# Kernel tuning notes

Hardware: AMD Instinct MI355X
Metric: run time of the kernel (lower is better)

The kernel has to match this reference:

```python
import jax, jax.numpy as jnp
import numpy as np

E = 256  # embed_dim (hardcoded in source module)
H = 4    # n_head
D = E // H
SEQ = 32768


def setup_inputs() -> dict:
    key = jax.random.key(0)
    ks = jax.random.split(key, 5)
    x = jax.random.normal(ks[0], (SEQ, E), dtype=jnp.float32)
    in_proj_weight = jax.random.normal(ks[1], (3 * E, E), dtype=jnp.float32) * (1.0 / np.sqrt(E))
    in_proj_bias = jax.random.normal(ks[2], (3 * E,), dtype=jnp.float32) * 0.02
    out_proj_weight = jax.random.normal(ks[3], (E, E), dtype=jnp.float32) * (1.0 / np.sqrt(E))
    out_proj_bias = jax.random.normal(ks[4], (E,), dtype=jnp.float32) * 0.02
    return {
        "x": x,
        "in_proj_weight": in_proj_weight,
        "in_proj_bias": in_proj_bias,
        "out_proj_weight": out_proj_weight,
        "out_proj_bias": out_proj_bias,
    }


def reference(x, in_proj_weight, in_proj_bias, out_proj_weight, out_proj_bias):
    # QKV projections (q uses only the first token of x: single-query decode attention)
    Wq, Wk, Wv = in_proj_weight[:E], in_proj_weight[E:2 * E], in_proj_weight[2 * E:]
    bq, bk, bv = in_proj_bias[:E], in_proj_bias[E:2 * E], in_proj_bias[2 * E:]
    q = x[:1] @ Wq.T + bq            # [1, E]
    k = x @ Wk.T + bk                # [S, E]
    v = x @ Wv.T + bv                # [S, E]

    qh = q.reshape(H, D)             # [H, D] (single query)
    kh = k.reshape(-1, H, D)         # [S, H, D]
    vh = v.reshape(-1, H, D)         # [S, H, D]

    scale = 1.0 / np.sqrt(D).astype(np.float32)
    scores = jnp.einsum("hd,shd->hs", qh, kh) * scale   # [H, S]
    attn = jax.nn.softmax(scores, axis=-1)                # [H, S]
    ctx = jnp.einsum("hs,shd->hd", attn, vh)             # [H, D]

    out = ctx.reshape(1, E) @ out_proj_weight.T + out_proj_bias  # [1, E]
    return out
```

## Files before the change

kernel.cpp:

```cpp
#include <hip/hip_runtime.h>
#include <hip/hip_cooperative_groups.h>
namespace cg = cooperative_groups;

#define NBLK 272
#define NB_B 256
#define WS_LP   0
#define WS_YV   1024
#define WS_B2   2048
#define WS_KQ   2304
#define WS_C4   3328
#define WS_M2   3392
#define WS_YP   265536

__device__ __forceinline__ float dot4(float4 a, float4 b) {
  return a.x * b.x + a.y * b.y + a.z * b.z + a.w * b.w;
}

__device__ __forceinline__ void phaseA_kq(const float* __restrict__ x, const float* __restrict__ W,
                                          const float* __restrict__ inb, float* __restrict__ kq,
                                          float* __restrict__ c4, float* sh, int ab, int t) {
  float* xs = sh;
  float* qls = sh + 256;
  float* red = sh + 320;
  const int lane = t & 63, w = t >> 6;
  const int h = ab >> 2, qt = ab & 3;
  if (t < 256) xs[t] = x[t];
  __syncthreads();
  const float4 xv = *(const float4*)&xs[lane * 4];
#pragma unroll
  for (int k = 0; k < 8; ++k) {
    const int eloc = w * 8 + k;
    const int row = h * 64 + eloc;
    float4 wv = *(const float4*)&W[(size_t)row * 256 + lane * 4];
    float p = dot4(wv, xv);
#pragma unroll
    for (int m = 1; m < 64; m <<= 1) p += __shfl_xor(p, m);
    if (lane == 0) qls[eloc] = p + inb[row];
  }
  __syncthreads();
  const int cl = t & 63, ds = t >> 6;
  float acc = 0.f;
#pragma unroll
  for (int d2 = 0; d2 < 8; ++d2) {
    const int d = ds * 8 + d2;
    acc += W[(size_t)(256 + h * 64 + d) * 256 + qt * 64 + cl] * qls[d];
  }
  red[ds * 64 + cl] = acc;
  __syncthreads();
  if (ds == 0) {
    float s = 0.f;
#pragma unroll
    for (int i = 0; i < 8; ++i) s += red[i * 64 + cl];
    kq[h * 256 + qt * 64 + cl] = s;
  }
  if (qt == 0 && t < 64) {
    float v = qls[t] * inb[256 + h * 64 + t];
#pragma unroll
    for (int m = 1; m < 64; m <<= 1) v += __shfl_xor(v, m);
    if (t == 0) c4[h] = v;
  }
}

__device__ __forceinline__ void phaseA_m2(const float* __restrict__ W, const float* __restrict__ Wout,
                                          float* __restrict__ M2, float* sh, int b2, int t) {
  float* wout_t = sh;
  const int tile = b2 >> 1, sub = b2 & 1;
  const int h = tile >> 4, e0 = (tile & 15) * 16 + sub * 8;
  {
    const int e = t >> 6, d = t & 63;
    wout_t[e * 64 + d] = Wout[(size_t)(e0 + e) * 256 + h * 64 + d];
  }
  __syncthreads();
  const int c = t & 255, eh = t >> 8;
  float acc[4] = {0.f, 0.f, 0.f, 0.f};
#pragma unroll 8
  for (int d = 0; d < 64; ++d) {
    const float wv = W[(size_t)(512 + h * 64 + d) * 256 + c];
#pragma unroll
    for (int e = 0; e < 4; ++e) acc[e] += wv * wout_t[(eh * 4 + e) * 64 + d];
  }
#pragma unroll
  for (int e = 0; e < 4; ++e)
    M2[(size_t)(e0 + eh * 4 + e) * 1024 + h * 256 + c] = acc[e];
}

__device__ __forceinline__ void phaseA_b2(const float* __restrict__ Wout, const float* __restrict__ inb,
                                          const float* __restrict__ bout, float* __restrict__ bias2,
                                          float* sh, int b, int t) {
  float* red = sh;
  const int og = t >> 5, seg = t & 31;
  const int e = b * 16 + og;
  float acc = 0.f;
#pragma unroll
  for (int j = 0; j < 8; ++j)
    acc += Wout[(size_t)e * 256 + seg * 8 + j] * inb[512 + seg * 8 + j];
  red[og * 32 + seg] = acc;
  __syncthreads();
  if (t < 16) {
    float s = bout[b * 16 + t];
#pragma unroll
    for (int i = 0; i < 32; ++i) s += red[t * 32 + i];
    bias2[b * 16 + t] = s;
  }
}

__device__ __forceinline__ float bscore(float4 xv, float4 kq0, float4 kq1, float4 kq2,
                                        float4 kq3, float c4v, int lane) {
  float p0 = dot4(xv, kq0), p1 = dot4(xv, kq1), p2 = dot4(xv, kq2), p3 = dot4(xv, kq3);
  const bool b1 = (lane & 2) != 0;
  float keep0 = b1 ? p2 : p0, send0 = b1 ? p0 : p2;
  keep0 += __shfl_xor(send0, 2);
  float keep1 = b1 ? p3 : p1, send1 = b1 ? p1 : p3;
  keep1 += __shfl_xor(send1, 2);
  const bool b0 = (lane & 1) != 0;
  float vv = b0 ? keep1 : keep0, sv = b0 ? keep0 : keep1;
  vv += __shfl_xor(sv, 1);
  vv += __shfl_xor(vv, 4);
  vv += __shfl_xor(vv, 8);
  vv += __shfl_xor(vv, 16);
  vv += __shfl_xor(vv, 32);
  return (vv + c4v) * 0.125f;
}

__device__ __forceinline__ void phaseB_core(const float4* xvA, const float4* xvB,
                                            const float* __restrict__ kq, const float* __restrict__ c4,
                                            float* __restrict__ ypart, float* __restrict__ lpart,
                                            float* yls, int bid, int t) {
  float* sll = yls + 8192;
  const int lane = t & 63, w = t >> 6;
  const int hme = lane & 3;
  const float4 kq0 = *(const float4*)&kq[0 * 256 + lane * 4];
  const float4 kq1 = *(const float4*)&kq[1 * 256 + lane * 4];
  const float4 kq2 = *(const float4*)&kq[2 * 256 + lane * 4];
  const float4 kq3 = *(const float4*)&kq[3 * 256 + lane * 4];
  const float c4v = c4[hme];

  float vA[8], vB[8];
#pragma unroll
  for (int r = 0; r < 8; ++r) vA[r] = bscore(xvA[r], kq0, kq1, kq2, kq3, c4v, lane);
#pragma unroll
  for (int r = 0; r < 8; ++r) vB[r] = bscore(xvB[r], kq0, kq1, kq2, kq3, c4v, lane);

  float l = 0.f;
  float4 a[4];
#pragma unroll
  for (int k = 0; k < 4; ++k) a[k] = (float4){0.f, 0.f, 0.f, 0.f};
#pragma unroll
  for (int r = 0; r < 8; ++r) {
    const float e0 = __expf(vA[r]);
    l += e0;
    const float e1 = __shfl_xor(e0, 1);
    const float e2 = __shfl_xor(e0, 2);
    const float e3 = __shfl_xor(e0, 3);
    a[0].x += e0 * xvA[r].x; a[0].y += e0 * xvA[r].y; a[0].z += e0 * xvA[r].z; a[0].w += e0 * xvA[r].w;
    a[1].x += e1 * xvA[r].x; a[1].y += e1 * xvA[r].y; a[1].z += e1 * xvA[r].z; a[1].w += e1 * xvA[r].w;
    a[2].x += e2 * xvA[r].x; a[2].y += e2 * xvA[r].y; a[2].z += e2 * xvA[r].z; a[2].w += e2 * xvA[r].w;
    a[3].x += e3 * xvA[r].x; a[3].y += e3 * xvA[r].y; a[3].z += e3 * xvA[r].z; a[3].w += e3 * xvA[r].w;
  }
#pragma unroll
  for (int r = 0; r < 8; ++r) {
    const float e0 = __expf(vB[r]);
    l += e0;
    const float e1 = __shfl_xor(e0, 1);
    const float e2 = __shfl_xor(e0, 2);
    const float e3 = __shfl_xor(e0, 3);
    a[0].x += e0 * xvB[r].x; a[0].y += e0 * xvB[r].y; a[0].z += e0 * xvB[r].z; a[0].w += e0 * xvB[r].w;
    a[1].x += e1 * xvB[r].x; a[1].y += e1 * xvB[r].y; a[1].z += e1 * xvB[r].z; a[1].w += e1 * xvB[r].w;
    a[2].x += e2 * xvB[r].x; a[2].y += e2 * xvB[r].y; a[2].z += e2 * xvB[r].z; a[2].w += e2 * xvB[r].w;
    a[3].x += e3 * xvB[r].x; a[3].y += e3 * xvB[r].y; a[3].z += e3 * xvB[r].z; a[3].w += e3 * xvB[r].w;
  }

  __syncthreads();
  if (lane < 4) sll[w * 4 + lane] = l;
#pragma unroll
  for (int k = 0; k < 4; ++k) {
    const int h = hme ^ k;
    *(float4*)&yls[w * 1024 + h * 256 + lane * 4] = a[k];
  }
  __syncthreads();

  if (t < 4) {
    float lb = 0.f;
#pragma unroll
    for (int i = 0; i < 8; ++i) lb += sll[i * 4 + t];
    lpart[t * NB_B + bid] = lb;
  }
  float* yp = &ypart[(size_t)bid * 1024];
#pragma unroll
  for (int o = t; o < 1024; o += 512) {
    float s = 0.f;
#pragma unroll
    for (int i = 0; i < 8; ++i) s += yls[i * 1024 + o];
    yp[o] = s;
  }
}

__device__ __forceinline__ void phaseC(const float* __restrict__ ypart, const float* __restrict__ lpart,
                                       float* __restrict__ z, float* sh, int bid, int t) {
  float* lred = sh;
  float* sred = sh + 256;
  const int h = bid >> 4;
  const int o0 = bid * 16;
  if (t < 256) lred[t] = lpart[h * 256 + t];
  __syncthreads();
  for (int s = 128; s > 0; s >>= 1) {
    if (t < s) lred[t] += lred[t + s];
    __syncthreads();
  }
  const float inv = 1.0f / lred[0];
  const int ol = t & 15, bg = t >> 4;
  float s = 0.f;
#pragma unroll
  for (int j = 0; j < 8; ++j) {
    const int b = bg * 8 + j;
    s += ypart[(size_t)b * 1024 + o0 + ol];
  }
  sred[bg * 16 + ol] = s;
  __syncthreads();
  if (t < 16) {
    float tot = 0.f;
#pragma unroll
    for (int g = 0; g < 32; ++g) tot += sred[g * 16 + t];
    z[o0 + t] = tot * inv;
  }
}

__device__ __forceinline__ void phaseD(const float* __restrict__ M2, const float* __restrict__ z,
                                       const float* __restrict__ bias2, float* __restrict__ out,
                                       float* sh, int bid, int t) {
  float* zls = sh;
  float* smo = sh + 1024;
  for (int i = t; i < 1024; i += 512) zls[i] = z[i];
  __syncthreads();
  const int og = t >> 5, seg = t & 31;
  const int e = bid * 16 + og;
  float acc = 0.f;
  const float4* m4 = (const float4*)&M2[(size_t)e * 1024 + seg * 32];
  const float4* z4 = (const float4*)&zls[seg * 32];
#pragma unroll
  for (int j = 0; j < 8; ++j) acc += dot4(m4[j], z4[j]);
  smo[og * 32 + seg] = acc;
  __syncthreads();
  if (t < 16) {
    float s = bias2[bid * 16 + t];
#pragma unroll
    for (int i = 0; i < 32; ++i) s += smo[t * 32 + i];
    out[bid * 16 + t] = s;
  }
}

__global__ void __launch_bounds__(512, 2) mha_coop(const float* __restrict__ x,
                                                   const float* __restrict__ W,
                                                   const float* __restrict__ inb,
                                                   const float* __restrict__ Wout,
                                                   const float* __restrict__ bout,
                                                   float* __restrict__ out,
                                                   float* __restrict__ ws) {
  __shared__ __align__(16) float sh[8224];
  const int t = threadIdx.x, bid = blockIdx.x;
  const int lane = t & 63, w = t >> 6;
  cg::grid_group grid = cg::this_grid();

  float4 xvA[8], xvB[8];

  if (bid < NB_B) {
    const int r0 = bid * 128 + w * 16;
#pragma unroll
    for (int r = 0; r < 8; ++r)
      xvA[r] = *(const float4*)&x[(size_t)(r0 + r) * 256 + lane * 4];
#pragma unroll
    for (int r = 0; r < 8; ++r)
      xvB[r] = *(const float4*)&x[(size_t)(r0 + 8 + r) * 256 + lane * 4];
  } else {
    phaseA_kq(x, W, inb, ws + WS_KQ, ws + WS_C4, sh, bid - NB_B, t);
  }

  grid.sync();
  if (bid < NB_B)
    phaseB_core(xvA, xvB, ws + WS_KQ, ws + WS_C4, ws + WS_YP, ws + WS_LP, sh, bid, t);
  grid.sync();
  if (bid < 64) phaseC(ws + WS_YP, ws + WS_LP, ws + WS_YV, sh, bid, t);
  else if (bid < 192) phaseA_m2(W, Wout, ws + WS_M2, sh, bid - 64, t);
  else if (bid < 208) phaseA_b2(Wout, inb, bout, ws + WS_B2, sh, bid - 192, t);
  grid.sync();
  if (bid < 16) phaseD(ws + WS_M2, ws + WS_YV, ws + WS_B2, out, sh, bid, t);
}

__global__ void __launch_bounds__(512) fb_A(const float* __restrict__ x, const float* __restrict__ W,
                                            const float* __restrict__ inb, float* __restrict__ ws) {
  __shared__ __align__(16) float sh[832];
  phaseA_kq(x, W, inb, ws + WS_KQ, ws + WS_C4, sh, blockIdx.x, threadIdx.x);
}
__global__ void __launch_bounds__(512) fb_B(const float* __restrict__ x, float* __restrict__ ws) {
  __shared__ __align__(16) float sh[8224];
  const int bid = blockIdx.x, t = threadIdx.x;
  const int lane = t & 63, w = t >> 6;
  const int r0 = bid * 128 + w * 16;
  float4 xvA[8], xvB[8];
#pragma unroll
  for (int r = 0; r < 8; ++r)
    xvA[r] = *(const float4*)&x[(size_t)(r0 + r) * 256 + lane * 4];
#pragma unroll
  for (int r = 0; r < 8; ++r)
    xvB[r] = *(const float4*)&x[(size_t)(r0 + 8 + r) * 256 + lane * 4];
  phaseB_core(xvA, xvB, ws + WS_KQ, ws + WS_C4, ws + WS_YP, ws + WS_LP, sh, bid, t);
}
__global__ void __launch_bounds__(512) fb_CM(const float* __restrict__ W, const float* __restrict__ Wout,
                                             const float* __restrict__ inb, const float* __restrict__ bout,
                                             float* __restrict__ ws) {
  __shared__ __align__(16) float sh[832];
  const int bid = blockIdx.x, t = threadIdx.x;
  if (bid < 64) phaseC(ws + WS_YP, ws + WS_LP, ws + WS_YV, sh, bid, t);
  else if (bid < 192) phaseA_m2(W, Wout, ws + WS_M2, sh, bid - 64, t);
  else if (bid < 208) phaseA_b2(Wout, inb, bout, ws + WS_B2, sh, bid - 192, t);
}
__global__ void __launch_bounds__(512) fb_D(float* __restrict__ out, float* __restrict__ ws) {
  __shared__ __align__(16) float sh[1536];
  phaseD(ws + WS_M2, ws + WS_YV, ws + WS_B2, out, sh, blockIdx.x, threadIdx.x);
}

extern "C" void kernel_launch(void* const* d_in, const int* in_sizes, int n_in,
                              void* d_out, int out_size, void* d_ws, size_t ws_size,
                              hipStream_t stream) {
  const float* x = (const float*)d_in[0];
  const float* W = (const float*)d_in[1];
  const float* inb = (const float*)d_in[2];
  const float* Wout = (const float*)d_in[3];
  const float* bout = (const float*)d_in[4];
  float* out = (float*)d_out;
  float* ws = (float*)d_ws;

  int dev = 0;
  (void)hipGetDevice(&dev);
  int coopAttr = 0, ncu = 0, occ = 0;
  bool coop = (hipDeviceGetAttribute(&coopAttr, hipDeviceAttributeCooperativeLaunch, dev) == hipSuccess) &&
              coopAttr != 0;
  coop = coop &&
         (hipDeviceGetAttribute(&ncu, hipDeviceAttributeMultiprocessorCount, dev) == hipSuccess);
  coop = coop &&
         (hipOccupancyMaxActiveBlocksPerMultiprocessor(&occ, mha_coop, 512, 0) == hipSuccess);
  coop = coop && (occ * ncu >= NBLK);

  if (coop) {
    void* args[] = {(void*)&x, (void*)&W, (void*)&inb, (void*)&Wout,
                    (void*)&bout, (void*)&out, (void*)&ws};
    if (hipLaunchCooperativeKernel((const void*)mha_coop, dim3(NBLK), dim3(512),
                                   args, 0, stream) == hipSuccess)
      return;
  }
  fb_A<<<16, 512, 0, stream>>>(x, W, inb, ws);
  fb_B<<<NB_B, 512, 0, stream>>>(x, ws);
  fb_CM<<<208, 512, 0, stream>>>(W, Wout, inb, bout, ws);
  fb_D<<<16, 512, 0, stream>>>(out, ws);
}
```

Measured before the change: 33.87 us.

## Distribute q/kq projection across all attention blocks and drop dedicated phase-A blocks

```diff
diff --git a/kernel.cpp b/kernel.cpp
--- a/kernel.cpp
+++ b/kernel.cpp
@@ -2,8 +2,7 @@
 #include <hip/hip_cooperative_groups.h>
 namespace cg = cooperative_groups;
 
-#define NBLK 272
-#define NB_B 256
+#define NBLK 256
 #define WS_LP   0
 #define WS_YV   1024
 #define WS_B2   2048
@@ -16,48 +15,34 @@
   return a.x * b.x + a.y * b.y + a.z * b.z + a.w * b.w;
 }
 
-__device__ __forceinline__ void phaseA_kq(const float* __restrict__ x, const float* __restrict__ W,
-                                          const float* __restrict__ inb, float* __restrict__ kq,
-                                          float* __restrict__ c4, float* sh, int ab, int t) {
-  float* xs = sh;
-  float* qls = sh + 256;
-  float* red = sh + 320;
+__device__ __forceinline__ void phaseA_dist(const float* __restrict__ x, const float* __restrict__ W,
+                                            const float* __restrict__ inb, float* __restrict__ kq,
+                                            float* __restrict__ c4, float* qls, int bid, int t) {
   const int lane = t & 63, w = t >> 6;
-  const int h = ab >> 2, qt = ab & 3;
-  if (t < 256) xs[t] = x[t];
-  __syncthreads();
-  const float4 xv = *(const float4*)&xs[lane * 4];
-#pragma unroll
-  for (int k = 0; k < 8; ++k) {
-    const int eloc = w * 8 + k;
-    const int row = h * 64 + eloc;
-    float4 wv = *(const float4*)&W[(size_t)row * 256 + lane * 4];
-    float p = dot4(wv, xv);
-#pragma unroll
-    for (int m = 1; m < 64; m <<= 1) p += __shfl_xor(p, m);
-    if (lane == 0) qls[eloc] = p + inb[row];
-  }
-  __syncthreads();
-  const int cl = t & 63, ds = t >> 6;
-  float acc = 0.f;
-#pragma unroll
-  for (int d2 = 0; d2 < 8; ++d2) {
-    const int d = ds * 8 + d2;
-    acc += W[(size_t)(256 + h * 64 + d) * 256 + qt * 64 + cl] * qls[d];
-  }
-  red[ds * 64 + cl] = acc;
-  __syncthreads();
-  if (ds == 0) {
-    float s = 0.f;
-#pragma unroll
-    for (int i = 0; i < 8; ++i) s += red[i * 64 + cl];
-    kq[h * 256 + qt * 64 + cl] = s;
-  }
-  if (qt == 0 && t < 64) {
-    float v = qls[t] * inb[256 + h * 64 + t];
+  const int h = bid >> 6;
+  const int c0 = (bid & 63) * 4;
+  const int rloc = lane >> 3, sub = lane & 7;
+  const int row = h * 64 + w * 8 + rloc;
+  const float4* w4 = (const float4*)&W[(size_t)row * 256 + sub * 32];
+  const float4* x4 = (const float4*)&x[sub * 32];
+  float p = 0.f;
+#pragma unroll
+  for (int j = 0; j < 8; ++j) p += dot4(w4[j], x4[j]);
+  p += __shfl_xor(p, 1);
+  p += __shfl_xor(p, 2);
+  p += __shfl_xor(p, 4);
+  if (sub == 0) qls[w * 8 + rloc] = p + inb[row];
+  __syncthreads();
+  if (w < 4) {
+    float v = W[(size_t)(256 + h * 64 + lane) * 256 + (c0 + w)] * qls[lane];
 #pragma unroll
     for (int m = 1; m < 64; m <<= 1) v += __shfl_xor(v, m);
-    if (t == 0) c4[h] = v;
+    if (lane == 0) kq[h * 256 + c0 + w] = v;
+  } else if (w == 4 && (bid & 63) == 0) {
+    float v = inb[256 + h * 64 + lane] * qls[lane];
+#pragma unroll
+    for (int m = 1; m < 64; m <<= 1) v += __shfl_xor(v, m);
+    if (lane == 0) c4[h] = v;
   }
 }
 
@@ -183,7 +168,7 @@
     float lb = 0.f;
 #pragma unroll
     for (int i = 0; i < 8; ++i) lb += sll[i * 4 + t];
-    lpart[t * NB_B + bid] = lb;
+    lpart[t * NBLK + bid] = lb;
   }
   float* yp = &ypart[(size_t)bid * 1024];
 #pragma unroll
@@ -249,7 +234,7 @@
   }
 }
 
-__global__ void __launch_bounds__(512, 2) mha_coop(const float* __restrict__ x,
+__global__ void __launch_bounds__(512, 1) mha_coop(const float* __restrict__ x,
                                                    const float* __restrict__ W,
                                                    const float* __restrict__ inb,
                                                    const float* __restrict__ Wout,
@@ -261,23 +246,19 @@
   const int lane = t & 63, w = t >> 6;
   cg::grid_group grid = cg::this_grid();
 
+  const int r0 = bid * 128 + w * 16;
   float4 xvA[8], xvB[8];
-
-  if (bid < NB_B) {
-    const int r0 = bid * 128 + w * 16;
-#pragma unroll
-    for (int r = 0; r < 8; ++r)
-      xvA[r] = *(const float4*)&x[(size_t)(r0 + r) * 256 + lane * 4];
-#pragma unroll
-    for (int r = 0; r < 8; ++r)
-      xvB[r] = *(const float4*)&x[(size_t)(r0 + 8 + r) * 256 + lane * 4];
-  } else {
-    phaseA_kq(x, W, inb, ws + WS_KQ, ws + WS_C4, sh, bid - NB_B, t);
-  }
+#pragma unroll
+  for (int r = 0; r < 8; ++r)
+    xvA[r] = *(const float4*)&x[(size_t)(r0 + r) * 256 + lane * 4];
+#pragma unroll
+  for (int r = 0; r < 8; ++r)
+    xvB[r] = *(const float4*)&x[(size_t)(r0 + 8 + r) * 256 + lane * 4];
+
+  phaseA_dist(x, W, inb, ws + WS_KQ, ws + WS_C4, sh, bid, t);
 
   grid.sync();
-  if (bid < NB_B)
-    phaseB_core(xvA, xvB, ws + WS_KQ, ws + WS_C4, ws + WS_YP, ws + WS_LP, sh, bid, t);
+  phaseB_core(xvA, xvB, ws + WS_KQ, ws + WS_C4, ws + WS_YP, ws + WS_LP, sh, bid, t);
   grid.sync();
   if (bid < 64) phaseC(ws + WS_YP, ws + WS_LP, ws + WS_YV, sh, bid, t);
   else if (bid < 192) phaseA_m2(W, Wout, ws + WS_M2, sh, bid - 64, t);
@@ -288,8 +269,8 @@
 
 __global__ void __launch_bounds__(512) fb_A(const float* __restrict__ x, const float* __restrict__ W,
                                             const float* __restrict__ inb, float* __restrict__ ws) {
-  __shared__ __align__(16) float sh[832];
-  phaseA_kq(x, W, inb, ws + WS_KQ, ws + WS_C4, sh, blockIdx.x, threadIdx.x);
+  __shared__ __align__(16) float sh[64];
+  phaseA_dist(x, W, inb, ws + WS_KQ, ws + WS_C4, sh, blockIdx.x, threadIdx.x);
 }
 __global__ void __launch_bounds__(512) fb_B(const float* __restrict__ x, float* __restrict__ ws) {
   __shared__ __align__(16) float sh[8224];
@@ -348,8 +329,8 @@
                                    args, 0, stream) == hipSuccess)
       return;
   }
-  fb_A<<<16, 512, 0, stream>>>(x, W, inb, ws);
-  fb_B<<<NB_B, 512, 0, stream>>>(x, ws);
+  fb_A<<<NBLK, 512, 0, stream>>>(x, W, inb, ws);
+  fb_B<<<NBLK, 512, 0, stream>>>(x, ws);
   fb_CM<<<208, 512, 0, stream>>>(W, Wout, inb, bout, ws);
   fb_D<<<16, 512, 0, stream>>>(out, ws);
 }
```

Result: faster. 31.79 us (median of 2 runs) (-6.1%).
